# Kernel tuning notes

Hardware: AMD Instinct MI355X
Metric: run time of the kernel (lower is better)

Reference implementation:

```python
import jax, jax.numpy as jnp
import numpy as np

N_NODES = 50000
N_EDGES = 800000
IN_DIM = 4
HID = 64
N_LAYERS = 3
BN_EPS = 1e-5


def setup_inputs() -> dict:
    key = jax.random.key(0)
    ks = jax.random.split(key, 16)
    x = jax.random.normal(ks[0], (N_NODES, IN_DIM), dtype=jnp.float32)
    edge_index = jax.random.randint(ks[1], (2, N_EDGES), 0, N_NODES, dtype=jnp.int32)
    # input projection
    W_in = jax.random.normal(ks[2], (IN_DIM, HID), dtype=jnp.float32) * 0.1
    b_in = jnp.zeros((HID,), dtype=jnp.float32)
    # stacked per-layer GCN weights and BatchNorm (eval-mode) params
    conv_w = jax.random.normal(ks[3], (N_LAYERS, HID, HID), dtype=jnp.float32) * 0.1
    conv_b = jnp.zeros((N_LAYERS, HID), dtype=jnp.float32)
    bn_gamma = jnp.ones((N_LAYERS, HID), dtype=jnp.float32)
    bn_beta = jnp.zeros((N_LAYERS, HID), dtype=jnp.float32)
    bn_mean = jax.random.normal(ks[4], (N_LAYERS, HID), dtype=jnp.float32) * 0.01
    bn_var = jnp.abs(jax.random.normal(ks[5], (N_LAYERS, HID), dtype=jnp.float32)) * 0.1 + 1.0
    # output projection: Linear(HID,HID) -> ReLU -> Dropout(eval: identity) -> Linear(HID,OUT)
    W1 = jax.random.normal(ks[6], (HID, HID), dtype=jnp.float32) * 0.1
    b1 = jnp.zeros((HID,), dtype=jnp.float32)
    W2 = jax.random.normal(ks[7], (HID, IN_DIM), dtype=jnp.float32) * 0.01  # xavier gain 0.1
    b2 = jnp.zeros((IN_DIM,), dtype=jnp.float32)
    return {
        "x": x, "edge_index": edge_index,
        "W_in": W_in, "b_in": b_in,
        "conv_w": conv_w, "conv_b": conv_b,
        "bn_gamma": bn_gamma, "bn_beta": bn_beta,
        "bn_mean": bn_mean, "bn_var": bn_var,
        "W1": W1, "b1": b1, "W2": W2, "b2": b2,
    }


def _gcn_graph(edge_index, n_nodes):
    """Add self loops and compute symmetric GCN normalization per edge."""
    loops = jnp.arange(n_nodes, dtype=edge_index.dtype)
    src = jnp.concatenate([edge_index[0], loops])
    dst = jnp.concatenate([edge_index[1], loops])
    deg = jax.ops.segment_sum(jnp.ones_like(dst, dtype=jnp.float32), dst,
                              num_segments=n_nodes)  # in-degree incl. self loop
    dinv = jax.lax.rsqrt(jnp.maximum(deg, 1e-12))
    enorm = dinv[src] * dinv[dst]  # [E+N]
    return src, dst, enorm


def reference(x, edge_index, W_in, b_in, conv_w, conv_b, bn_gamma, bn_beta,
              bn_mean, bn_var, W1, b1, W2, b2):
    n = x.shape[0]
    src, dst, enorm = _gcn_graph(edge_index, n)

    input_x = x
    h = x @ W_in + b_in  # [N, HID]
    for i in range(N_LAYERS):
        residual = h
        # GCNConv: linear -> normalized gather/scatter aggregate -> bias
        hw = h @ conv_w[i]
        msg = hw[src] * enorm[:, None]  # [E+N, HID] irregular gather
        h = jax.ops.segment_sum(msg, dst, num_segments=n) + conv_b[i]
        # BatchNorm1d (eval) + ReLU (dropout is identity in eval)
        h = (h - bn_mean[i]) * jax.lax.rsqrt(bn_var[i] + BN_EPS) * bn_gamma[i] + bn_beta[i]
        h = jax.nn.relu(h)
        h = h + residual  # shapes always match (HID == HID)
    # output projection MLP
    delta = jax.nn.relu(h @ W1 + b1) @ W2 + b2  # [N, IN_DIM]
    return input_x + delta
```

## Files before the change

### kernel.cpp

```cpp
#include <hip/hip_runtime.h>

#define HID 64

__device__ __forceinline__ float bf2f(unsigned short u) {
    return __uint_as_float(((unsigned)u) << 16);
}
__device__ __forceinline__ unsigned short f2bf(float f) {
    unsigned u = __float_as_uint(f);
    u += 0x7FFF + ((u >> 16) & 1);
    return (unsigned short)(u >> 16);
}

__global__ void hist_part(const int* __restrict__ dst, int* __restrict__ counts,
                          int E, int nodes_per, int chunk) {
    int p = blockIdx.x & 7;
    int q = blockIdx.x >> 3;
    int lo = p * nodes_per;
    int hi = lo + nodes_per;
    int beg = q * chunk;
    int end = min(beg + chunk, E);
    for (int e = beg + threadIdx.x; e < end; e += 256) {
        int d = dst[e];
        if (d >= lo && d < hi) atomicAdd(&counts[d], 1);
    }
}

__global__ void scan1(const int* __restrict__ counts, int* __restrict__ tmp,
                      int* __restrict__ bsum, float* __restrict__ dinv, int n) {
    __shared__ int s[256];
    int t = threadIdx.x;
    int i = blockIdx.x * 256 + t;
    int v = (i < n) ? counts[i] : 0;
    if (i < n) dinv[i] = rsqrtf((float)v + 1.0f);
    s[t] = v;
    __syncthreads();
#pragma unroll
    for (int d = 1; d < 256; d <<= 1) {
        int x = (t >= d) ? s[t - d] : 0;
        __syncthreads();
        s[t] += x;
        __syncthreads();
    }
    if (i < n) tmp[i] = s[t];
    if (t == 255) bsum[blockIdx.x] = s[255];
}

__global__ void scan3b(const int* __restrict__ counts, const int* __restrict__ tmp,
                       const int* __restrict__ bsum, int* __restrict__ rowptr,
                       int* __restrict__ cursor, int n, int nb) {
    __shared__ int sb[256];
    int t = threadIdx.x;
    int b = blockIdx.x;
    sb[t] = (t < b && t < nb) ? bsum[t] : 0;
    __syncthreads();
#pragma unroll
    for (int d = 128; d > 0; d >>= 1) {
        if (t < d) sb[t] += sb[t + d];
        __syncthreads();
    }
    int boffb = sb[0];
    int i = b * 256 + t;
    if (i < n) {
        int r = tmp[i] - counts[i] + boffb;
        rowptr[i] = r;
        cursor[i] = r;
    }
    if (i == n - 1) rowptr[n] = tmp[i] + boffb;
}

__global__ void fill_gemm(const int* __restrict__ eidx, int* __restrict__ cursor,
                          int* __restrict__ col, int E, int n, int nodes_per,
                          int chunk, int fillBlocks,
                          const float* __restrict__ x, const float* __restrict__ Win,
                          const float* __restrict__ bin, const float* __restrict__ W,
                          const float* __restrict__ dinv, float* __restrict__ h,
                          unsigned short* __restrict__ hws) {
    if (blockIdx.x < fillBlocks) {
        int p = blockIdx.x & 7;
        int q = blockIdx.x >> 3;
        const int* __restrict__ dst = eidx + E;
        int lo = p * nodes_per;
        int hi = lo + nodes_per;
        int beg = q * chunk;
        int end = min(beg + chunk, E);
        for (int e = beg + threadIdx.x; e < end; e += 256) {
            int d = dst[e];
            if (d >= lo && d < hi) {
                int s = eidx[e];
                int pos = atomicAdd(&cursor[d], 1);
                col[pos] = s;
            }
        }
        return;
    }
    __shared__ float wl[64 * 64];
    __shared__ float winl[256];
    __shared__ float binl[64];
    __shared__ float hl[256];
    int b = blockIdx.x - fillBlocks;
    int tid = threadIdx.x;
#pragma unroll
    for (int i = 0; i < 16; ++i) wl[tid + 256 * i] = W[tid + 256 * i];
    winl[tid] = Win[tid];
    if (tid < 64) binl[tid] = bin[tid];
    int j = tid & 63;
    int w = tid >> 6;
    for (int c = 0; c < 8; ++c) {
        int v = b * 32 + c * 4 + w;
        __syncthreads();
        float hv = 0.f;
        if (v < n) {
            float4 xv = *(const float4*)&x[(size_t)v * 4];
            hv = binl[j] + xv.x * winl[j] + xv.y * winl[64 + j]
                         + xv.z * winl[128 + j] + xv.w * winl[192 + j];
            h[(size_t)v * 64 + j] = hv;
        }
        hl[tid] = hv;
        __syncthreads();
        if (v < n) {
            const float* hr = &hl[w * 64];
            float acc = 0.f;
#pragma unroll
            for (int k = 0; k < 64; ++k) acc += hr[k] * wl[k * 64 + j];
            hws[(size_t)v * 64 + j] = f2bf(acc * dinv[v]);
        }
    }
}

#define GATHER_BODY(hws4, col, beg, end, s0, s1, s2, s3, gl)                      \
    {                                                                             \
        int e = beg;                                                              \
        for (; e + 7 < end; e += 8) {                                             \
            int c0 = col[e], c1 = col[e+1], c2 = col[e+2], c3 = col[e+3];         \
            int c4 = col[e+4], c5 = col[e+5], c6 = col[e+6], c7 = col[e+7];       \
            ushort4 m0 = hws4[(size_t)c0 * 16 + gl];                              \
            ushort4 m1 = hws4[(size_t)c1 * 16 + gl];                              \
            ushort4 m2 = hws4[(size_t)c2 * 16 + gl];                              \
            ushort4 m3 = hws4[(size_t)c3 * 16 + gl];                              \
            ushort4 m4 = hws4[(size_t)c4 * 16 + gl];                              \
            ushort4 m5 = hws4[(size_t)c5 * 16 + gl];                              \
            ushort4 m6 = hws4[(size_t)c6 * 16 + gl];                              \
            ushort4 m7 = hws4[(size_t)c7 * 16 + gl];                              \
            s0 += bf2f(m0.x)+bf2f(m1.x)+bf2f(m2.x)+bf2f(m3.x)                     \
                + bf2f(m4.x)+bf2f(m5.x)+bf2f(m6.x)+bf2f(m7.x);                    \
            s1 += bf2f(m0.y)+bf2f(m1.y)+bf2f(m2.y)+bf2f(m3.y)                     \
                + bf2f(m4.y)+bf2f(m5.y)+bf2f(m6.y)+bf2f(m7.y);                    \
            s2 += bf2f(m0.z)+bf2f(m1.z)+bf2f(m2.z)+bf2f(m3.z)                     \
                + bf2f(m4.z)+bf2f(m5.z)+bf2f(m6.z)+bf2f(m7.z);                    \
            s3 += bf2f(m0.w)+bf2f(m1.w)+bf2f(m2.w)+bf2f(m3.w)                     \
                + bf2f(m4.w)+bf2f(m5.w)+bf2f(m6.w)+bf2f(m7.w);                    \
        }                                                                         \
        for (; e + 3 < end; e += 4) {                                             \
            int c0 = col[e], c1 = col[e+1], c2 = col[e+2], c3 = col[e+3];         \
            ushort4 m0 = hws4[(size_t)c0 * 16 + gl];                              \
            ushort4 m1 = hws4[(size_t)c1 * 16 + gl];                              \
            ushort4 m2 = hws4[(size_t)c2 * 16 + gl];                              \
            ushort4 m3 = hws4[(size_t)c3 * 16 + gl];                              \
            s0 += bf2f(m0.x)+bf2f(m1.x)+bf2f(m2.x)+bf2f(m3.x);                    \
            s1 += bf2f(m0.y)+bf2f(m1.y)+bf2f(m2.y)+bf2f(m3.y);                    \
            s2 += bf2f(m0.z)+bf2f(m1.z)+bf2f(m2.z)+bf2f(m3.z);                    \
            s3 += bf2f(m0.w)+bf2f(m1.w)+bf2f(m2.w)+bf2f(m3.w);                    \
        }                                                                         \
        for (; e < end; ++e) {                                                    \
            ushort4 me = hws4[(size_t)col[e] * 16 + gl];                          \
            s0 += bf2f(me.x); s1 += bf2f(me.y); s2 += bf2f(me.z); s3 += bf2f(me.w);\
        }                                                                         \
    }

__global__ void gather_gemm(const int* __restrict__ rowptr, const int* __restrict__ col,
                            const unsigned short* __restrict__ hws_in,
                            const float* __restrict__ dinv, float* __restrict__ h,
                            const float* __restrict__ cb, const float* __restrict__ gamma,
                            const float* __restrict__ beta, const float* __restrict__ mean,
                            const float* __restrict__ var, const float* __restrict__ Wn,
                            unsigned short* __restrict__ hws_out, int n) {
    __shared__ float wl[64 * 64];
    __shared__ float hl[16 * 64];
    int tid = threadIdx.x;
#pragma unroll
    for (int i = 0; i < 16; ++i) wl[tid + 256 * i] = Wn[tid + 256 * i];
    int lane = tid & 63, wave = tid >> 6;
    int grp = lane >> 4, gl = lane & 15;
    int ln = wave * 4 + grp;
    int v = blockIdx.x * 16 + ln;
    bool valid = v < n;
    int vv = valid ? v : 0;
    int j0 = gl * 4;
    const ushort4* hws4 = (const ushort4*)hws_in;
    ushort4 m = hws4[(size_t)vv * 16 + gl];
    float s0 = bf2f(m.x), s1 = bf2f(m.y), s2 = bf2f(m.z), s3 = bf2f(m.w);
    int beg = rowptr[vv];
    int end = valid ? rowptr[vv + 1] : beg;
    GATHER_BODY(hws4, col, beg, end, s0, s1, s2, s3, gl)
    float di = dinv[vv];
    float4 cbv = *(const float4*)&cb[j0];
    float4 mnv = *(const float4*)&mean[j0];
    float4 vrv = *(const float4*)&var[j0];
    float4 gmv = *(const float4*)&gamma[j0];
    float4 btv = *(const float4*)&beta[j0];
    float4 hres = *(const float4*)&h[(size_t)vv * 64 + j0];
    float4 o;
    o.x = fmaxf((s0 * di + cbv.x - mnv.x) * rsqrtf(vrv.x + 1e-5f) * gmv.x + btv.x, 0.f) + hres.x;
    o.y = fmaxf((s1 * di + cbv.y - mnv.y) * rsqrtf(vrv.y + 1e-5f) * gmv.y + btv.y, 0.f) + hres.y;
    o.z = fmaxf((s2 * di + cbv.z - mnv.z) * rsqrtf(vrv.z + 1e-5f) * gmv.z + btv.z, 0.f) + hres.z;
    o.w = fmaxf((s3 * di + cbv.w - mnv.w) * rsqrtf(vrv.w + 1e-5f) * gmv.w + btv.w, 0.f) + hres.w;
    if (valid) *(float4*)&h[(size_t)vv * 64 + j0] = o;
    *(float4*)&hl[ln * 64 + j0] = o;
    __syncthreads();
    int j = lane;
    for (int c = 0; c < 4; ++c) {
        int ln2 = wave * 4 + c;
        int v2 = blockIdx.x * 16 + ln2;
        if (v2 < n) {
            const float* hr = &hl[ln2 * 64];
            float acc = 0.f;
#pragma unroll
            for (int k = 0; k < 64; ++k) acc += hr[k] * wl[k * 64 + j];
            hws_out[(size_t)v2 * 64 + j] = f2bf(acc * dinv[v2]);
        }
    }
}

__global__ void gather_mlp(const int* __restrict__ rowptr, const int* __restrict__ col,
                           const unsigned short* __restrict__ hws_in,
                           const float* __restrict__ dinv, const float* __restrict__ h,
                           const float* __restrict__ cb, const float* __restrict__ gamma,
                           const float* __restrict__ beta, const float* __restrict__ mean,
                           const float* __restrict__ var, const float* __restrict__ x,
                           const float* __restrict__ W1, const float* __restrict__ b1,
                           const float* __restrict__ W2, const float* __restrict__ b2,
                           float* __restrict__ out, int n) {
    __shared__ float wl[64 * 64];
    __shared__ float w2l[256];
    __shared__ float hl[16 * 64];
    __shared__ float tl[16 * 68];
    int tid = threadIdx.x;
#pragma unroll
    for (int i = 0; i < 16; ++i) wl[tid + 256 * i] = W1[tid + 256 * i];
    w2l[tid] = W2[tid];
    int lane = tid & 63, wave = tid >> 6;
    int grp = lane >> 4, gl = lane & 15;
    int ln = wave * 4 + grp;
    int v = blockIdx.x * 16 + ln;
    bool valid = v < n;
    int vv = valid ? v : 0;
    int j0 = gl * 4;
    const ushort4* hws4 = (const ushort4*)hws_in;
    ushort4 m = hws4[(size_t)vv * 16 + gl];
    float s0 = bf2f(m.x), s1 = bf2f(m.y), s2 = bf2f(m.z), s3 = bf2f(m.w);
    int beg = rowptr[vv];
    int end = valid ? rowptr[vv + 1] : beg;
    GATHER_BODY(hws4, col, beg, end, s0, s1, s2, s3, gl)
    float di = dinv[vv];
    float4 cbv = *(const float4*)&cb[j0];
    float4 mnv = *(const float4*)&mean[j0];
    float4 vrv = *(const float4*)&var[j0];
    float4 gmv = *(const float4*)&gamma[j0];
    float4 btv = *(const float4*)&beta[j0];
    float4 hres = *(const float4*)&h[(size_t)vv * 64 + j0];
    float4 o;
    o.x = fmaxf((s0 * di + cbv.x - mnv.x) * rsqrtf(vrv.x + 1e-5f) * gmv.x + btv.x, 0.f) + hres.x;
    o.y = fmaxf((s1 * di + cbv.y - mnv.y) * rsqrtf(vrv.y + 1e-5f) * gmv.y + btv.y, 0.f) + hres.y;
    o.z = fmaxf((s2 * di + cbv.z - mnv.z) * rsqrtf(vrv.z + 1e-5f) * gmv.z + btv.z, 0.f) + hres.z;
    o.w = fmaxf((s3 * di + cbv.w - mnv.w) * rsqrtf(vrv.w + 1e-5f) * gmv.w + btv.w, 0.f) + hres.w;
    *(float4*)&hl[ln * 64 + j0] = o;
    __syncthreads();
    int j = lane;
    float b1j = b1[j];
    for (int c = 0; c < 4; ++c) {
        int ln2 = wave * 4 + c;
        const float* hr = &hl[ln2 * 64];
        float acc = b1j;
#pragma unroll
        for (int k = 0; k < 64; ++k) acc += hr[k] * wl[k * 64 + j];
        tl[ln2 * 68 + j] = fmaxf(acc, 0.f);
    }
    __syncthreads();
    if (tid < 64) {
        int ln2 = tid >> 2, mm = tid & 3;
        int v2 = blockIdx.x * 16 + ln2;
        if (v2 < n) {
            const float* tr = &tl[ln2 * 68];
            float acc = b2[mm];
#pragma unroll
            for (int k = 0; k < 64; ++k) acc += tr[k] * w2l[k * 4 + mm];
            out[(size_t)v2 * 4 + mm] = x[(size_t)v2 * 4 + mm] + acc;
        }
    }
}

extern "C" void kernel_launch(void* const* d_in, const int* in_sizes, int n_in,
                              void* d_out, int out_size, void* d_ws, size_t ws_size,
                              hipStream_t stream) {
    const float* x     = (const float*)d_in[0];
    const int*   eidx  = (const int*)  d_in[1];
    const float* Win   = (const float*)d_in[2];
    const float* bin   = (const float*)d_in[3];
    const float* convw = (const float*)d_in[4];
    const float* convb = (const float*)d_in[5];
    const float* gamma = (const float*)d_in[6];
    const float* beta  = (const float*)d_in[7];
    const float* mean  = (const float*)d_in[8];
    const float* var   = (const float*)d_in[9];
    const float* W1    = (const float*)d_in[10];
    const float* b1    = (const float*)d_in[11];
    const float* W2    = (const float*)d_in[12];
    const float* b2    = (const float*)d_in[13];
    float* out = (float*)d_out;

    int n = in_sizes[0] / 4;
    int E = in_sizes[1] / 2;
    const int B = 256;
    int NB = (n + B - 1) / B;

    char* p = (char*)d_ws;
    size_t nh = (size_t)n * 64;
    float*          dinv   = (float*)p;          p += ((size_t)n + 16) * 4;
    float*          h      = (float*)p;          p += nh * 4;
    unsigned short* hws0   = (unsigned short*)p; p += nh * 2;
    unsigned short* hws1   = (unsigned short*)p; p += nh * 2;
    int*            counts = (int*)p;            p += (size_t)n * 4;
    int*            cursor = (int*)p;            p += (size_t)n * 4;
    int*            tmp    = (int*)p;            p += (size_t)n * 4;
    int*            rowptr = (int*)p;            p += ((size_t)n + 16) * 4;
    int*            bsum   = (int*)p;            p += 256 * 4;
    int*            col    = (int*)p;            p += (size_t)E * 4;

    const int GP = 128;
    int fillBlocks = GP * 8;
    int nodes_per = (n + 7) / 8;
    int chunk = (E + GP - 1) / GP;

    hipMemsetAsync(counts, 0, (size_t)n * 4, stream);
    hist_part<<<fillBlocks, B, 0, stream>>>(eidx + E, counts, E, nodes_per, chunk);
    scan1<<<NB, B, 0, stream>>>(counts, tmp, bsum, dinv, n);
    scan3b<<<NB, B, 0, stream>>>(counts, tmp, bsum, rowptr, cursor, n, NB);

    int NB32 = (n + 31) / 32;
    fill_gemm<<<fillBlocks + NB32, B, 0, stream>>>(
        eidx, cursor, col, E, n, nodes_per, chunk, fillBlocks,
        x, Win, bin, convw, dinv, h, hws0);

    int NB16 = (n + 15) / 16;
    gather_gemm<<<NB16, B, 0, stream>>>(rowptr, col, hws0, dinv, h,
        convb, gamma, beta, mean, var, convw + 4096, hws1, n);
    gather_gemm<<<NB16, B, 0, stream>>>(rowptr, col, hws1, dinv, h,
        convb + 64, gamma + 64, beta + 64, mean + 64, var + 64, convw + 8192, hws0, n);
    gather_mlp<<<NB16, B, 0, stream>>>(rowptr, col, hws0, dinv, h,
        convb + 128, gamma + 128, beta + 128, mean + 128, var + 128,
        x, W1, b1, W2, b2, out, n);
}
```

Baseline: 272.8 us.

## Fuse two-pass prefix scan into single-pass scan with inter-block flag spinning

Replaces the two scan kernels with one kernel where each block publishes its block sum, offset by one so that zero means not ready, and spins on the sums of earlier blocks to get its offset. This drops one launch and the tmp array round-trip, and bsum is now cleared by the enlarged memset. It relies on all 196 blocks being co-resident, or at least scheduled in order, to avoid deadlock. Stores of h and hws in fill_gemm are also made nontemporal to reduce cache pollution.

Result: no change. 275.8 us (+1.1%).

```diff
diff --git a/kernel.cpp b/kernel.cpp
--- a/kernel.cpp
+++ b/kernel.cpp
@@ -25,11 +25,14 @@
     }
 }
 
-__global__ void scan1(const int* __restrict__ counts, int* __restrict__ tmp,
-                      int* __restrict__ bsum, float* __restrict__ dinv, int n) {
+__global__ void scan_fused(const int* __restrict__ counts, int* __restrict__ bsum,
+                           int* __restrict__ rowptr, int* __restrict__ cursor,
+                           float* __restrict__ dinv, int n) {
     __shared__ int s[256];
+    __shared__ int pre[256];
     int t = threadIdx.x;
-    int i = blockIdx.x * 256 + t;
+    int b = blockIdx.x;
+    int i = b * 256 + t;
     int v = (i < n) ? counts[i] : 0;
     if (i < n) dinv[i] = rsqrtf((float)v + 1.0f);
     s[t] = v;
@@ -41,31 +44,27 @@
         s[t] += x;
         __syncthreads();
     }
-    if (i < n) tmp[i] = s[t];
-    if (t == 255) bsum[blockIdx.x] = s[255];
-}
-
-__global__ void scan3b(const int* __restrict__ counts, const int* __restrict__ tmp,
-                       const int* __restrict__ bsum, int* __restrict__ rowptr,
-                       int* __restrict__ cursor, int n, int nb) {
-    __shared__ int sb[256];
-    int t = threadIdx.x;
-    int b = blockIdx.x;
-    sb[t] = (t < b && t < nb) ? bsum[t] : 0;
+    if (t == 255) atomicExch(&bsum[b], s[255] + 1);
+    int myp = 0;
+    if (t < b) {
+        int val;
+        do { val = atomicAdd(&bsum[t], 0); } while (val == 0);
+        myp = val - 1;
+    }
+    pre[t] = myp;
     __syncthreads();
 #pragma unroll
     for (int d = 128; d > 0; d >>= 1) {
-        if (t < d) sb[t] += sb[t + d];
-        __syncthreads();
-    }
-    int boffb = sb[0];
-    int i = b * 256 + t;
+        if (t < d) pre[t] += pre[t + d];
+        __syncthreads();
+    }
+    int boffb = pre[0];
     if (i < n) {
-        int r = tmp[i] - counts[i] + boffb;
+        int r = s[t] - v + boffb;
         rowptr[i] = r;
         cursor[i] = r;
     }
-    if (i == n - 1) rowptr[n] = tmp[i] + boffb;
+    if (i == n - 1) rowptr[n] = s[t] + boffb;
 }
 
 __global__ void fill_gemm(const int* __restrict__ eidx, int* __restrict__ cursor,
@@ -113,7 +112,7 @@
             float4 xv = *(const float4*)&x[(size_t)v * 4];
             hv = binl[j] + xv.x * winl[j] + xv.y * winl[64 + j]
                          + xv.z * winl[128 + j] + xv.w * winl[192 + j];
-            h[(size_t)v * 64 + j] = hv;
+            __builtin_nontemporal_store(hv, &h[(size_t)v * 64 + j]);
         }
         hl[tid] = hv;
         __syncthreads();
@@ -122,7 +121,7 @@
             float acc = 0.f;
 #pragma unroll
             for (int k = 0; k < 64; ++k) acc += hr[k] * wl[k * 64 + j];
-            hws[(size_t)v * 64 + j] = f2bf(acc * dinv[v]);
+            __builtin_nontemporal_store(f2bf(acc * dinv[v]), &hws[(size_t)v * 64 + j]);
         }
     }
 }
@@ -320,10 +319,9 @@
     unsigned short* hws0   = (unsigned short*)p; p += nh * 2;
     unsigned short* hws1   = (unsigned short*)p; p += nh * 2;
     int*            counts = (int*)p;            p += (size_t)n * 4;
+    int*            bsum   = (int*)p;            p += 256 * 4;
     int*            cursor = (int*)p;            p += (size_t)n * 4;
-    int*            tmp    = (int*)p;            p += (size_t)n * 4;
     int*            rowptr = (int*)p;            p += ((size_t)n + 16) * 4;
-    int*            bsum   = (int*)p;            p += 256 * 4;
     int*            col    = (int*)p;            p += (size_t)E * 4;
 
     const int GP = 128;
@@ -331,10 +329,9 @@
     int nodes_per = (n + 7) / 8;
     int chunk = (E + GP - 1) / GP;
 
-    hipMemsetAsync(counts, 0, (size_t)n * 4, stream);
+    hipMemsetAsync(counts, 0, ((size_t)n + 256) * 4, stream);
     hist_part<<<fillBlocks, B, 0, stream>>>(eidx + E, counts, E, nodes_per, chunk);
-    scan1<<<NB, B, 0, stream>>>(counts, tmp, bsum, dinv, n);
-    scan3b<<<NB, B, 0, stream>>>(counts, tmp, bsum, rowptr, cursor, n, NB);
+    scan_fused<<<NB, B, 0, stream>>>(counts, bsum, rowptr, cursor, dinv, n);
 
     int NB32 = (n + 31) / 32;
     fill_gemm<<<fillBlocks + NB32, B, 0, stream>>>(
```
